# Optimization experiments

Hardware: AMD Instinct MI355X
Metric: run time of the kernel (lower is better)

Reference implementation:

```python
import jax, jax.numpy as jnp
import numpy as np

B, H, W, C = 2, 64, 64, 512
GROUPS = 32
EPS = 1e-5


def group_norm(x, gamma, beta):
    b, h, w, c = x.shape
    xg = x.reshape(b, h, w, GROUPS, c // GROUPS)
    mu = xg.mean(axis=(1, 2, 4), keepdims=True)
    var = xg.var(axis=(1, 2, 4), keepdims=True)
    xn = ((xg - mu) * jax.lax.rsqrt(var + EPS)).reshape(b, h, w, c)
    return xn * gamma + beta


def setup_inputs() -> dict:
    key = jax.random.key(0)
    ks = jax.random.split(key, 12)
    wscale = 0.02
    inputs = jax.random.normal(ks[0], (B, H, W, C), jnp.float32)
    gamma = jnp.ones((C,), jnp.float32)
    beta = jnp.zeros((C,), jnp.float32)
    Wq = jax.random.normal(ks[1], (C, C), jnp.float32) * wscale
    bq = jnp.zeros((C,), jnp.float32)
    Wk = jax.random.normal(ks[2], (C, C), jnp.float32) * wscale
    bk = jnp.zeros((C,), jnp.float32)
    Wv = jax.random.normal(ks[3], (C, C), jnp.float32) * wscale
    bv = jnp.zeros((C,), jnp.float32)
    Wp = jax.random.normal(ks[4], (C, C), jnp.float32) * wscale
    bp = jnp.zeros((C,), jnp.float32)
    return {"inputs": inputs, "gamma": gamma, "beta": beta,
            "Wq": Wq, "bq": bq, "Wk": Wk, "bk": bk,
            "Wv": Wv, "bv": bv, "Wp": Wp, "bp": bp}


def reference(inputs, gamma, beta, Wq, bq, Wk, bk, Wv, bv, Wp, bp):
    b, h, w, c = inputs.shape
    x = group_norm(inputs, gamma, beta)
    # QKV projections on [b, h, w, c], flatten spatial to sequence hw
    q = (x @ Wq + bq).reshape(b, h * w, c)
    k = (x @ Wk + bk).reshape(b, h * w, c)
    v = (x @ Wv + bv).reshape(b, h * w, c)
    scale = 1.0 / jnp.sqrt(jnp.asarray(c, q.dtype))
    # y[b,i,j] = <q_i, k_j> / sqrt(c); softmax over keys j (last axis, keras default)
    attn = jax.nn.softmax(jnp.einsum('bqc,bkc->bqk', q, k) * scale, axis=-1)
    # out_i = sum_j attn[i,j] * v_j  (matches v @ y^T in the original)
    o = jnp.einsum('bqk,bkc->bqc', attn, v).reshape(b, h, w, c)
    return (o @ Wp + bp) + inputs
```

## Files before the change

kernel.cpp:

```cpp
#include <hip/hip_runtime.h>
#include <hip/hip_bf16.h>
#include <cstddef>


typedef __bf16 bf16;
typedef __attribute__((ext_vector_type(8))) __bf16 bf16x8;
typedef __attribute__((ext_vector_type(4))) __bf16 bf16x4;
typedef __attribute__((ext_vector_type(4))) float f32x4;

#define SEQ   4096
#define CCH   512
#define NBAT  2

__global__ __launch_bounds__(256) void prep(
    const float* __restrict__ x,
    const float* __restrict__ Wq, const float* __restrict__ Wk,
    const float* __restrict__ Wv, const float* __restrict__ Wp,
    const float* __restrict__ bq, const float* __restrict__ bk,
    const float* __restrict__ bv,
    float* __restrict__ stats, bf16* __restrict__ WqkvT,
    bf16* __restrict__ WpT, float* __restrict__ biasQKV) {
    const int bid = blockIdx.x;
    if (bid < 512) {
        int bg = bid >> 3, c = bid & 7;
        int b = bg >> 5, g = bg & 31;
        const float* base = x + (size_t)b * SEQ * CCH + g * 16;
        float s = 0.f, ss = 0.f;
        for (int i = threadIdx.x; i < 2048; i += 256) {
            int sp = c * 512 + (i >> 2), q = i & 3;
            float4 v = *(const float4*)(base + (size_t)sp * CCH + q * 4);
            s  += v.x + v.y + v.z + v.w;
            ss += v.x * v.x + v.y * v.y + v.z * v.z + v.w * v.w;
        }
        #pragma unroll
        for (int o = 32; o > 0; o >>= 1) { s += __shfl_down(s, o); ss += __shfl_down(ss, o); }
        __shared__ float red[2][4];
        int wave = threadIdx.x >> 6, lane = threadIdx.x & 63;
        if (lane == 0) { red[0][wave] = s; red[1][wave] = ss; }
        __syncthreads();
        if (threadIdx.x == 0) {
            atomicAdd(&stats[bg * 2],     red[0][0] + red[0][1] + red[0][2] + red[0][3]);
            atomicAdd(&stats[bg * 2 + 1], red[1][0] + red[1][1] + red[1][2] + red[1][3]);
        }
    } else if (bid < 1536) {
        __shared__ float tile[32][33];
        int w = bid - 512;
        int z = w >> 8, rest = w & 255;
        int k0 = (rest >> 4) * 32, n0 = (rest & 15) * 32;
        const float* W = (z == 0) ? Wq : (z == 1) ? Wk : (z == 2) ? Wv : Wp;
        int tx = threadIdx.x & 31, ty = threadIdx.x >> 5;
        #pragma unroll
        for (int i = ty; i < 32; i += 8)
            tile[i][tx] = W[(size_t)(k0 + i) * CCH + n0 + tx];
        __syncthreads();
        bf16* dst = (z < 3) ? (WqkvT + (size_t)z * CCH * CCH) : WpT;
        #pragma unroll
        for (int i = ty; i < 32; i += 8)
            dst[(size_t)(n0 + i) * CCH + k0 + tx] = (bf16)tile[tx][i];
    } else {
        for (int i = threadIdx.x; i < 1536; i += 256) {
            float v = (i < 512) ? bq[i] : (i < 1024) ? bk[i - 512] : bv[i - 1024];
            biasQKV[i] = v;
        }
    }
}

__global__ __launch_bounds__(256) void gn_apply(const float* __restrict__ x,
                                                const float* __restrict__ stats,
                                                const float* __restrict__ gamma,
                                                const float* __restrict__ beta,
                                                bf16* __restrict__ xn) {
    size_t idx = (size_t)blockIdx.x * 256 + threadIdx.x;
    int c4 = (int)(idx & 127);
    size_t sb = idx >> 7;
    int b = (int)(sb >> 12);
    int g = c4 >> 2;
    int bg = b * 32 + g;
    float S = stats[bg * 2], SS = stats[bg * 2 + 1];
    float mu = S * (1.f / 65536.f);
    float rs = rsqrtf(SS * (1.f / 65536.f) - mu * mu + 1e-5f);
    float4 v  = ((const float4*)x)[idx];
    float4 gm = ((const float4*)gamma)[c4];
    float4 bt = ((const float4*)beta)[c4];
    bf16x4 o;
    o[0] = (bf16)((v.x - mu) * rs * gm.x + bt.x);
    o[1] = (bf16)((v.y - mu) * rs * gm.y + bt.y);
    o[2] = (bf16)((v.z - mu) * rs * gm.z + bt.z);
    o[3] = (bf16)((v.w - mu) * rs * gm.w + bt.w);
    ((bf16x4*)xn)[idx] = o;
}

template <int EPI, int BN>
__device__ __forceinline__ void gemm2_body(
    int bxi, int byi, int bzi,
    const bf16* __restrict__ A, long long aBatch, int lda,
    const bf16* __restrict__ Bt, long long bBatch, int ldb,
    void* __restrict__ Cout, long long cBatch, int ldc,
    int K, int bkmask, float scale,
    const float* __restrict__ bias, const float* __restrict__ resid,
    float* __restrict__ lsum, long long lsumBatch) {
    constexpr int JN = BN / 32;
    __shared__ __align__(16) bf16 As[128 * 64];
    __shared__ __align__(16) bf16 Bs[BN * 64];
    __shared__ float lscr[256];
    __shared__ float lrow[128];
    const int tid = threadIdx.x;
    const int lane = tid & 63;
    const int wave = tid >> 6;

    int zb = bzi, kc = 0;
    if constexpr (EPI == 2) { kc = zb & 1; zb >>= 1; }
    const long long m0 = (long long)bxi * 128;
    const long long n0 = (long long)byi * BN;
    const bf16* Ab = A + (long long)zb * aBatch + (EPI == 2 ? (long long)kc * 2048 : 0);
    const bf16* Bb = Bt + (long long)zb * bBatch + (EPI == 2 ? (long long)kc * 2048 : 0);

    if constexpr (EPI == 2) {
        const float* lsb = lsum + (long long)zb * lsumBatch + m0;
        const int row = tid & 127, h = tid >> 7;
        float s = 0.f;
        #pragma unroll
        for (int p = 0; p < 32; ++p)
            s += lsb[(long long)(h * 32 + p) * SEQ + row];
        lscr[tid] = s;
        __syncthreads();
        if (tid < 128) lrow[tid] = 1.f / (lscr[tid] + lscr[tid + 128]);
    }

    const int wm = (wave & 1) * 64;
    const int wn = (wave >> 1) * (BN / 2);
    const int fm = lane & 15;
    const int q4 = lane >> 4;

    f32x4 acc[4][JN];
    #pragma unroll
    for (int i = 0; i < 4; ++i)
        #pragma unroll
        for (int j = 0; j < JN; ++j)
            acc[i][j] = (f32x4){0.f, 0.f, 0.f, 0.f};

    const int srow = tid >> 3;
    const int schunk = (tid & 7) ^ (srow & 7);

    for (int k0 = 0; k0 < K; k0 += 64) {
        const int kA = k0 + schunk * 8;
        const int kB = (k0 & bkmask) + schunk * 8;
        #pragma unroll
        for (int cb = 0; cb < 4; ++cb) {
            const bf16* g = Ab + (m0 + cb * 32 + srow) * (long long)lda + kA;
            __builtin_amdgcn_global_load_lds((const __attribute__((address_space(1))) void*)g,
                                             (__attribute__((address_space(3))) void*)&As[cb * 2048 + tid * 8], 16, 0, 0);
        }
        #pragma unroll
        for (int cb = 0; cb < BN / 32; ++cb) {
            const bf16* g = Bb + (n0 + cb * 32 + srow) * (long long)ldb + kB;
            __builtin_amdgcn_global_load_lds((const __attribute__((address_space(1))) void*)g,
                                             (__attribute__((address_space(3))) void*)&Bs[cb * 2048 + tid * 8], 16, 0, 0);
        }
        __syncthreads();
        #pragma unroll
        for (int kcc = 0; kcc < 2; ++kcc) {
            bf16x8 fa[4], fb[JN];
            #pragma unroll
            for (int i = 0; i < 4; ++i) {
                const int row = wm + i * 16 + fm;
                const int sw = ((kcc * 4 + q4) ^ (fm & 7)) * 8;
                fa[i] = *(const bf16x8*)&As[row * 64 + sw];
            }
            #pragma unroll
            for (int j = 0; j < JN; ++j) {
                const int row = wn + j * 16 + fm;
                const int sw = ((kcc * 4 + q4) ^ (fm & 7)) * 8;
                fb[j] = *(const bf16x8*)&Bs[row * 64 + sw];
            }
            #pragma unroll
            for (int i = 0; i < 4; ++i)
                #pragma unroll
                for (int j = 0; j < JN; ++j)
                    acc[i][j] = __builtin_amdgcn_mfma_f32_16x16x32_bf16(fa[i], fb[j], acc[i][j], 0, 0, 0);
        }
        __syncthreads();
    }

    const int col = lane & 15;
    const int rowb = (lane >> 4) * 4;

    if constexpr (EPI == 1) {
        bf16* Pb = (bf16*)Cout + (long long)zb * cBatch;
        float* lsw = lsum + (long long)zb * lsumBatch
                   + ((long long)byi * 2 + (wave >> 1)) * SEQ;
        #pragma unroll
        for (int i = 0; i < 4; ++i) {
            float rs[4] = {0.f, 0.f, 0.f, 0.f};
            long long mg = m0 + wm + i * 16 + rowb;
            #pragma unroll
            for (int j = 0; j < JN; ++j) {
                long long ng = n0 + wn + j * 16 + col;
                #pragma unroll
                for (int r = 0; r < 4; ++r) {
                    float e = __expf(acc[i][j][r] * scale);
                    rs[r] += e;
                    Pb[(mg + r) * (long long)ldc + ng] = (bf16)e;
                }
            }
            #pragma unroll
            for (int r = 0; r < 4; ++r) {
                rs[r] += __shfl_xor(rs[r], 1);
                rs[r] += __shfl_xor(rs[r], 2);
                rs[r] += __shfl_xor(rs[r], 4);
                rs[r] += __shfl_xor(rs[r], 8);
            }
            if (col == 0) {
                #pragma unroll
                for (int r = 0; r < 4; ++r) lsw[mg + r] = rs[r];
            }
        }
    } else {
        #pragma unroll
        for (int i = 0; i < 4; ++i) {
            #pragma unroll
            for (int j = 0; j < JN; ++j) {
                long long mg = m0 + wm + i * 16 + rowb;
                long long ng = n0 + wn + j * 16 + col;
                #pragma unroll
                for (int r = 0; r < 4; ++r) {
                    float v = acc[i][j][r];
                    long long m = mg + r;
                    if constexpr (EPI == 0) {
                        ((bf16*)Cout)[m * (long long)ldc + ng] = (bf16)(v + bias[ng]);
                    } else if constexpr (EPI == 2) {
                        float inv = lrow[(int)(m - m0)];
                        ((bf16*)Cout)[(long long)zb * cBatch + m * (long long)ldc
                                      + kc * 512 + ng] = (bf16)(v * inv);
                    } else {
                        ((float*)Cout)[m * (long long)ldc + ng] =
                            v + bias[ng] + resid[m * CCH + ng];
                    }
                }
            }
        }
    }
}

template <int EPI, int BN>
__global__ __launch_bounds__(256, 2) void gemm2(
    const bf16* __restrict__ A, long long aBatch, int lda,
    const bf16* __restrict__ Bt, long long bBatch, int ldb,
    void* __restrict__ Cout, long long cBatch, int ldc,
    int K, int bkmask, float scale,
    const float* __restrict__ bias, const float* __restrict__ resid,
    float* __restrict__ lsum, long long lsumBatch) {
    gemm2_body<EPI, BN>(blockIdx.x, blockIdx.y, blockIdx.z,
                        A, aBatch, lda, Bt, bBatch, ldb, Cout, cBatch, ldc,
                        K, bkmask, scale, bias, resid, lsum, lsumBatch);
}

__device__ __forceinline__ void vtrans_body(const bf16* __restrict__ qkv,
                                            bf16* __restrict__ vT,
                                            int b, int s0, int c0) {
    __shared__ bf16 tile[64][65];
    const int tx = threadIdx.x & 63;
    const int w = threadIdx.x >> 6;
    #pragma unroll
    for (int i = 0; i < 16; ++i) {
        int row = w + i * 4;
        tile[row][tx] = qkv[((size_t)b * SEQ + s0 + row) * 1536 + 1024 + c0 + tx];
    }
    __syncthreads();
    #pragma unroll
    for (int i = 0; i < 16; ++i) {
        int row = w + i * 4;
        vT[((size_t)b * CCH + c0 + row) * SEQ + s0 + tx] = tile[tx][row];
    }
}

__global__ __launch_bounds__(256, 2) void qk_vtrans(
    const bf16* __restrict__ qkv, bf16* __restrict__ vT,
    bf16* __restrict__ P, float* __restrict__ lsum,
    float scale, int vtBlocks,
    long long qkBatch, long long pBatch, long long lsumBatch) {
    const int bid = blockIdx.x;
    if (bid < vtBlocks) {
        int b = bid >> 9;
        int r = bid & 511;
        vtrans_body(qkv, vT, b, (r >> 3) * 64, (r & 7) * 64);
    } else {
        int q = bid - vtBlocks;
        int bz = q >> 10;
        int r = q & 1023;
        gemm2_body<1, 128>(r >> 5, r & 31, bz,
                           qkv, qkBatch, 1536, qkv + 512, qkBatch, 1536,
                           P, pBatch, SEQ, CCH, 0x7FFFFFFF, scale,
                           nullptr, nullptr, lsum, lsumBatch);
    }
}

extern "C" void kernel_launch(void* const* d_in, const int* in_sizes, int n_in,
                              void* d_out, int out_size, void* d_ws, size_t ws_size,
                              hipStream_t stream) {
    const float* x     = (const float*)d_in[0];
    const float* gamma = (const float*)d_in[1];
    const float* beta  = (const float*)d_in[2];
    const float* Wq    = (const float*)d_in[3];
    const float* bq    = (const float*)d_in[4];
    const float* Wk    = (const float*)d_in[5];
    const float* bk    = (const float*)d_in[6];
    const float* Wv    = (const float*)d_in[7];
    const float* bv    = (const float*)d_in[8];
    const float* Wp    = (const float*)d_in[9];
    const float* bp    = (const float*)d_in[10];
    float* out = (float*)d_out;

    constexpr size_t OFF_STATS = 0;
    constexpr size_t OFF_BIAS  = 1024;
    constexpr size_t OFF_WQKVT = 8192;
    constexpr size_t OFF_WPT   = 1581056;
    constexpr size_t OFF_XN    = 2105344;
    constexpr size_t OFF_LSUM  = OFF_XN;
    constexpr size_t OFF_QKV   = 10493952;
    constexpr size_t OFF_O2    = OFF_QKV;
    constexpr size_t OFF_VT    = 35659776;
    constexpr size_t OFF_P     = 44048384;
    constexpr size_t NEED_FULL = OFF_P + (size_t)NBAT * SEQ * SEQ * 2;

    char* ws = (char*)d_ws;
    float* stats   = (float*)(ws + OFF_STATS);
    float* biasQKV = (float*)(ws + OFF_BIAS);
    bf16*  WqkvT   = (bf16*)(ws + OFF_WQKVT);
    bf16*  WpT     = (bf16*)(ws + OFF_WPT);
    bf16*  xn      = (bf16*)(ws + OFF_XN);
    float* lsum    = (float*)(ws + OFF_LSUM);
    bf16*  qkv     = (bf16*)(ws + OFF_QKV);
    bf16*  o2      = (bf16*)(ws + OFF_O2);
    bf16*  vT      = (bf16*)(ws + OFF_VT);
    bf16*  P       = (bf16*)(ws + OFF_P);

    const float scale = 0.044194173824159216f;
    const int NOMASK = 0x7FFFFFFF;

    hipMemsetAsync(ws + OFF_STATS, 0, 512, stream);
    prep<<<1537, 256, 0, stream>>>(x, Wq, Wk, Wv, Wp, bq, bk, bv,
                                   stats, WqkvT, WpT, biasQKV);
    gn_apply<<<4096, 256, 0, stream>>>(x, stats, gamma, beta, xn);
    gemm2<0, 128><<<dim3(64, 12, 1), 256, 0, stream>>>(
        xn, 0, CCH, WqkvT, 0, CCH, qkv, 0, 1536,
        CCH, NOMASK, 1.f, biasQKV, nullptr, nullptr, 0);

    if (ws_size >= NEED_FULL) {
        qk_vtrans<<<3072, 256, 0, stream>>>(
            qkv, vT, P, lsum, scale, 1024,
            (long long)SEQ * 1536, (long long)SEQ * SEQ, 64LL * SEQ);
        gemm2<2, 128><<<dim3(32, 4, NBAT * 2), 256, 0, stream>>>(
            P, (long long)SEQ * SEQ, SEQ, vT, (long long)CCH * SEQ, SEQ,
            o2, (long long)SEQ * 1024, 1024,
            2048, NOMASK, 1.f, nullptr, nullptr, lsum, 64LL * SEQ);
    } else {
        for (int b = 0; b < NBAT; ++b) {
            const bf16* qb = qkv + (long long)b * SEQ * 1536;
            qk_vtrans<<<1536, 256, 0, stream>>>(
                qb, vT + (long long)b * CCH * SEQ, P,
                lsum + (long long)b * 64 * SEQ, scale, 512, 0, 0, 0);
            gemm2<2, 128><<<dim3(32, 4, 2), 256, 0, stream>>>(
                P, 0, SEQ, vT + (long long)b * CCH * SEQ, 0, SEQ,
                o2 + (long long)b * SEQ * 1024, 0, 1024,
                2048, NOMASK, 1.f, nullptr, nullptr,
                lsum + (long long)b * 64 * SEQ, 0);
        }
    }

    gemm2<3, 64><<<dim3(64, 8, 1), 256, 0, stream>>>(
        o2, 0, 1024, WpT, 0, CCH, out, 0, CCH,
        1024, 511, 1.f, bp, x, nullptr, 0);
}
```

Baseline: 220.8 us.

## Fuse all stages into one persistent cooperative kernel with grid syncs

Replaces the sequence of separate kernel launches (memset, prep, group-norm apply, QKV GEMM, QK^T/V-transpose, PV GEMM, output projection) with a single cooperative kernel of 512 blocks that loops over work units per stage and uses grid-wide barriers between stages. The stats atomics and memset are replaced by per-chunk partial sums reduced once into a shared-memory mu/rstd table. Shared memory is unified into one buffer, and the PV epilogue's row-sum load now runs after the main loop. This targets launch gaps and the memset, at the cost of grid-sync overhead and persistent-loop scheduling with fixed occupancy.

```diff
diff --git a/kernel.cpp b/kernel.cpp
--- a/kernel.cpp
+++ b/kernel.cpp
@@ -1,6 +1,9 @@
 #include <hip/hip_runtime.h>
 #include <hip/hip_bf16.h>
+#include <hip/hip_cooperative_groups.h>
 #include <cstddef>
+
+namespace cg = cooperative_groups;
 
 
 typedef __bf16 bf16;
@@ -11,22 +14,25 @@
 #define SEQ   4096
 #define CCH   512
 #define NBAT  2
-
-__global__ __launch_bounds__(256) void prep(
-    const float* __restrict__ x,
+#define NOMASK 0x7FFFFFFF
+#define SMEM_BYTES 32768
+
+__device__ __forceinline__ void prep_unit(
+    char* smem, int bid, const float* __restrict__ x,
     const float* __restrict__ Wq, const float* __restrict__ Wk,
     const float* __restrict__ Wv, const float* __restrict__ Wp,
     const float* __restrict__ bq, const float* __restrict__ bk,
     const float* __restrict__ bv,
-    float* __restrict__ stats, bf16* __restrict__ WqkvT,
+    float* __restrict__ statsP, bf16* __restrict__ WqkvT,
     bf16* __restrict__ WpT, float* __restrict__ biasQKV) {
-    const int bid = blockIdx.x;
+    const int tid = threadIdx.x;
     if (bid < 512) {
+        float* red = (float*)smem;
         int bg = bid >> 3, c = bid & 7;
         int b = bg >> 5, g = bg & 31;
         const float* base = x + (size_t)b * SEQ * CCH + g * 16;
         float s = 0.f, ss = 0.f;
-        for (int i = threadIdx.x; i < 2048; i += 256) {
+        for (int i = tid; i < 2048; i += 256) {
             int sp = c * 512 + (i >> 2), q = i & 3;
             float4 v = *(const float4*)(base + (size_t)sp * CCH + q * 4);
             s  += v.x + v.y + v.z + v.w;
@@ -34,21 +40,21 @@
         }
         #pragma unroll
         for (int o = 32; o > 0; o >>= 1) { s += __shfl_down(s, o); ss += __shfl_down(ss, o); }
-        __shared__ float red[2][4];
-        int wave = threadIdx.x >> 6, lane = threadIdx.x & 63;
-        if (lane == 0) { red[0][wave] = s; red[1][wave] = ss; }
-        __syncthreads();
-        if (threadIdx.x == 0) {
-            atomicAdd(&stats[bg * 2],     red[0][0] + red[0][1] + red[0][2] + red[0][3]);
-            atomicAdd(&stats[bg * 2 + 1], red[1][0] + red[1][1] + red[1][2] + red[1][3]);
-        }
+        int wave = tid >> 6, lane = tid & 63;
+        if (lane == 0) { red[wave] = s; red[4 + wave] = ss; }
+        __syncthreads();
+        if (tid == 0) {
+            statsP[bg * 16 + c]     = red[0] + red[1] + red[2] + red[3];
+            statsP[bg * 16 + 8 + c] = red[4] + red[5] + red[6] + red[7];
+        }
+        __syncthreads();
     } else if (bid < 1536) {
-        __shared__ float tile[32][33];
+        float (*tile)[33] = (float(*)[33])smem;
         int w = bid - 512;
         int z = w >> 8, rest = w & 255;
         int k0 = (rest >> 4) * 32, n0 = (rest & 15) * 32;
         const float* W = (z == 0) ? Wq : (z == 1) ? Wk : (z == 2) ? Wv : Wp;
-        int tx = threadIdx.x & 31, ty = threadIdx.x >> 5;
+        int tx = tid & 31, ty = tid >> 5;
         #pragma unroll
         for (int i = ty; i < 32; i += 8)
             tile[i][tx] = W[(size_t)(k0 + i) * CCH + n0 + tx];
@@ -57,28 +63,39 @@
         #pragma unroll
         for (int i = ty; i < 32; i += 8)
             dst[(size_t)(n0 + i) * CCH + k0 + tx] = (bf16)tile[tx][i];
+        __syncthreads();
     } else {
-        for (int i = threadIdx.x; i < 1536; i += 256) {
+        for (int i = tid; i < 1536; i += 256) {
             float v = (i < 512) ? bq[i] : (i < 1024) ? bk[i - 512] : bv[i - 1024];
             biasQKV[i] = v;
         }
     }
 }
 
-__global__ __launch_bounds__(256) void gn_apply(const float* __restrict__ x,
-                                                const float* __restrict__ stats,
-                                                const float* __restrict__ gamma,
-                                                const float* __restrict__ beta,
-                                                bf16* __restrict__ xn) {
-    size_t idx = (size_t)blockIdx.x * 256 + threadIdx.x;
+__device__ __forceinline__ void gn_table(char* smem, const float* __restrict__ statsP) {
+    float* tbl = (float*)smem;
+    const int tid = threadIdx.x;
+    if (tid < 64) {
+        float S = 0.f, SS = 0.f;
+        #pragma unroll
+        for (int c = 0; c < 8; ++c) { S += statsP[tid * 16 + c]; SS += statsP[tid * 16 + 8 + c]; }
+        float mu = S * (1.f / 65536.f);
+        float rs = rsqrtf(SS * (1.f / 65536.f) - mu * mu + 1e-5f);
+        tbl[tid * 2] = mu; tbl[tid * 2 + 1] = rs;
+    }
+    __syncthreads();
+}
+
+__device__ __forceinline__ void gn_unit(
+    char* smem, int w, const float* __restrict__ x,
+    const float* __restrict__ gamma, const float* __restrict__ beta,
+    bf16* __restrict__ xn) {
+    const float* tbl = (const float*)smem;
+    size_t idx = (size_t)w * 256 + threadIdx.x;
     int c4 = (int)(idx & 127);
-    size_t sb = idx >> 7;
-    int b = (int)(sb >> 12);
-    int g = c4 >> 2;
-    int bg = b * 32 + g;
-    float S = stats[bg * 2], SS = stats[bg * 2 + 1];
-    float mu = S * (1.f / 65536.f);
-    float rs = rsqrtf(SS * (1.f / 65536.f) - mu * mu + 1e-5f);
+    int b = (int)(idx >> 19);
+    int bg = b * 32 + (c4 >> 2);
+    float mu = tbl[bg * 2], rs = tbl[bg * 2 + 1];
     float4 v  = ((const float4*)x)[idx];
     float4 gm = ((const float4*)gamma)[c4];
     float4 bt = ((const float4*)beta)[c4];
@@ -90,9 +107,30 @@
     ((bf16x4*)xn)[idx] = o;
 }
 
+__device__ __forceinline__ void vtrans_unit(char* smem,
+                                            const bf16* __restrict__ qkv,
+                                            bf16* __restrict__ vT,
+                                            int b, int s0, int c0) {
+    bf16 (*tile)[65] = (bf16(*)[65])smem;
+    const int tx = threadIdx.x & 63;
+    const int w = threadIdx.x >> 6;
+    #pragma unroll
+    for (int i = 0; i < 16; ++i) {
+        int row = w + i * 4;
+        tile[row][tx] = qkv[((size_t)b * SEQ + s0 + row) * 1536 + 1024 + c0 + tx];
+    }
+    __syncthreads();
+    #pragma unroll
+    for (int i = 0; i < 16; ++i) {
+        int row = w + i * 4;
+        vT[((size_t)b * CCH + c0 + row) * SEQ + s0 + tx] = tile[tx][row];
+    }
+    __syncthreads();
+}
+
 template <int EPI, int BN>
 __device__ __forceinline__ void gemm2_body(
-    int bxi, int byi, int bzi,
+    char* smem, int bxi, int byi, int bzi,
     const bf16* __restrict__ A, long long aBatch, int lda,
     const bf16* __restrict__ Bt, long long bBatch, int ldb,
     void* __restrict__ Cout, long long cBatch, int ldc,
@@ -100,10 +138,8 @@
     const float* __restrict__ bias, const float* __restrict__ resid,
     float* __restrict__ lsum, long long lsumBatch) {
     constexpr int JN = BN / 32;
-    __shared__ __align__(16) bf16 As[128 * 64];
-    __shared__ __align__(16) bf16 Bs[BN * 64];
-    __shared__ float lscr[256];
-    __shared__ float lrow[128];
+    bf16* As = (bf16*)smem;
+    bf16* Bs = (bf16*)(smem + 16384);
     const int tid = threadIdx.x;
     const int lane = tid & 63;
     const int wave = tid >> 6;
@@ -115,18 +151,6 @@
     const bf16* Ab = A + (long long)zb * aBatch + (EPI == 2 ? (long long)kc * 2048 : 0);
     const bf16* Bb = Bt + (long long)zb * bBatch + (EPI == 2 ? (long long)kc * 2048 : 0);
 
-    if constexpr (EPI == 2) {
-        const float* lsb = lsum + (long long)zb * lsumBatch + m0;
-        const int row = tid & 127, h = tid >> 7;
-        float s = 0.f;
-        #pragma unroll
-        for (int p = 0; p < 32; ++p)
-            s += lsb[(long long)(h * 32 + p) * SEQ + row];
-        lscr[tid] = s;
-        __syncthreads();
-        if (tid < 128) lrow[tid] = 1.f / (lscr[tid] + lscr[tid + 128]);
-    }
-
     const int wm = (wave & 1) * 64;
     const int wn = (wave >> 1) * (BN / 2);
     const int fm = lane & 15;
@@ -179,6 +203,21 @@
                 for (int j = 0; j < JN; ++j)
                     acc[i][j] = __builtin_amdgcn_mfma_f32_16x16x32_bf16(fa[i], fb[j], acc[i][j], 0, 0, 0);
         }
+        __syncthreads();
+    }
+
+    float* lrow = (float*)(smem + 1024);
+    if constexpr (EPI == 2) {
+        float* lscr = (float*)smem;
+        const float* lsb = lsum + (long long)zb * lsumBatch + m0;
+        const int row = tid & 127, h = tid >> 7;
+        float s = 0.f;
+        #pragma unroll
+        for (int p = 0; p < 32; ++p)
+            s += lsb[(long long)(h * 32 + p) * SEQ + row];
+        lscr[tid] = s;
+        __syncthreads();
+        if (tid < 128) lrow[tid] = 1.f / (lscr[tid] + lscr[tid + 128]);
         __syncthreads();
     }
 
@@ -242,55 +281,112 @@
     }
 }
 
+struct FusedArgs {
+    const float *x, *gamma, *beta, *Wq, *bq, *Wk, *bk, *Wv, *bv, *Wp, *bp;
+    float* out;
+    float* statsP; float* biasQKV; bf16* WqkvT; bf16* WpT; bf16* xn;
+    float* lsum; bf16* qkv; bf16* o2; bf16* vT; bf16* P;
+};
+
+__global__ __launch_bounds__(256, 2) void fused(FusedArgs a) {
+    cg::grid_group grid = cg::this_grid();
+    __shared__ __align__(16) char smem[SMEM_BYTES];
+    const int nb = gridDim.x;
+    const float scale = 0.044194173824159216f;
+
+    for (int w = blockIdx.x; w < 1537; w += nb)
+        prep_unit(smem, w, a.x, a.Wq, a.Wk, a.Wv, a.Wp, a.bq, a.bk, a.bv,
+                  a.statsP, a.WqkvT, a.WpT, a.biasQKV);
+    grid.sync();
+
+    gn_table(smem, a.statsP);
+    for (int w = blockIdx.x; w < 4096; w += nb)
+        gn_unit(smem, w, a.x, a.gamma, a.beta, a.xn);
+    grid.sync();
+
+    for (int w = blockIdx.x; w < 768; w += nb)
+        gemm2_body<0, 128>(smem, w & 63, w >> 6, 0,
+                           a.xn, 0, CCH, a.WqkvT, 0, CCH, a.qkv, 0, 1536,
+                           CCH, NOMASK, 1.f, a.biasQKV, nullptr, nullptr, 0);
+    grid.sync();
+
+    for (int w = blockIdx.x; w < 3072; w += nb) {
+        if (w < 1024) {
+            int b = w >> 9, r = w & 511;
+            vtrans_unit(smem, a.qkv, a.vT, b, (r >> 3) * 64, (r & 7) * 64);
+        } else {
+            int u = w - 1024;
+            int bz = u >> 10, r = u & 1023;
+            gemm2_body<1, 128>(smem, r >> 5, r & 31, bz,
+                               a.qkv, (long long)SEQ * 1536, 1536,
+                               a.qkv + 512, (long long)SEQ * 1536, 1536,
+                               a.P, (long long)SEQ * SEQ, SEQ,
+                               CCH, NOMASK, scale, nullptr, nullptr,
+                               a.lsum, 64LL * SEQ);
+        }
+    }
+    grid.sync();
+
+    for (int w = blockIdx.x; w < 512; w += nb)
+        gemm2_body<2, 128>(smem, w & 31, (w >> 5) & 3, w >> 7,
+                           a.P, (long long)SEQ * SEQ, SEQ,
+                           a.vT, (long long)CCH * SEQ, SEQ,
+                           a.o2, (long long)SEQ * 1024, 1024,
+                           2048, NOMASK, 1.f, nullptr, nullptr,
+                           a.lsum, 64LL * SEQ);
+    grid.sync();
+
+    for (int w = blockIdx.x; w < 512; w += nb)
+        gemm2_body<3, 64>(smem, w & 63, w >> 6, 0,
+                          a.o2, 0, 1024, a.WpT, 0, CCH, a.out, 0, CCH,
+                          1024, 511, 1.f, a.bp, a.x, nullptr, 0);
+}
+
+__global__ __launch_bounds__(256) void k_prep(
+    const float* x, const float* Wq, const float* Wk, const float* Wv,
+    const float* Wp, const float* bq, const float* bk, const float* bv,
+    float* statsP, bf16* WqkvT, bf16* WpT, float* biasQKV) {
+    __shared__ __align__(16) char smem[4352];
+    prep_unit(smem, blockIdx.x, x, Wq, Wk, Wv, Wp, bq, bk, bv,
+              statsP, WqkvT, WpT, biasQKV);
+}
+
+__global__ __launch_bounds__(256) void k_gn(
+    const float* x, const float* statsP, const float* gamma,
+    const float* beta, bf16* xn) {
+    __shared__ __align__(16) char smem[512];
+    gn_table(smem, statsP);
+    gn_unit(smem, blockIdx.x, x, gamma, beta, xn);
+}
+
 template <int EPI, int BN>
-__global__ __launch_bounds__(256, 2) void gemm2(
-    const bf16* __restrict__ A, long long aBatch, int lda,
-    const bf16* __restrict__ Bt, long long bBatch, int ldb,
-    void* __restrict__ Cout, long long cBatch, int ldc,
+__global__ __launch_bounds__(256, 2) void k_gemm2(
+    const bf16* A, long long aBatch, int lda,
+    const bf16* Bt, long long bBatch, int ldb,
+    void* Cout, long long cBatch, int ldc,
     int K, int bkmask, float scale,
-    const float* __restrict__ bias, const float* __restrict__ resid,
-    float* __restrict__ lsum, long long lsumBatch) {
-    gemm2_body<EPI, BN>(blockIdx.x, blockIdx.y, blockIdx.z,
+    const float* bias, const float* resid,
+    float* lsum, long long lsumBatch) {
+    __shared__ __align__(16) char smem[SMEM_BYTES];
+    gemm2_body<EPI, BN>(smem, blockIdx.x, blockIdx.y, blockIdx.z,
                         A, aBatch, lda, Bt, bBatch, ldb, Cout, cBatch, ldc,
                         K, bkmask, scale, bias, resid, lsum, lsumBatch);
 }
 
-__device__ __forceinline__ void vtrans_body(const bf16* __restrict__ qkv,
-                                            bf16* __restrict__ vT,
-                                            int b, int s0, int c0) {
-    __shared__ bf16 tile[64][65];
-    const int tx = threadIdx.x & 63;
-    const int w = threadIdx.x >> 6;
-    #pragma unroll
-    for (int i = 0; i < 16; ++i) {
-        int row = w + i * 4;
-        tile[row][tx] = qkv[((size_t)b * SEQ + s0 + row) * 1536 + 1024 + c0 + tx];
-    }
-    __syncthreads();
-    #pragma unroll
-    for (int i = 0; i < 16; ++i) {
-        int row = w + i * 4;
-        vT[((size_t)b * CCH + c0 + row) * SEQ + s0 + tx] = tile[tx][row];
-    }
-}
-
-__global__ __launch_bounds__(256, 2) void qk_vtrans(
-    const bf16* __restrict__ qkv, bf16* __restrict__ vT,
-    bf16* __restrict__ P, float* __restrict__ lsum,
-    float scale, int vtBlocks,
-    long long qkBatch, long long pBatch, long long lsumBatch) {
+__global__ __launch_bounds__(256, 2) void k_qk_vtrans(
+    const bf16* qkv, bf16* vT, bf16* P, float* lsum, float scale,
+    int vtBlocks, long long qkBatch, long long pBatch, long long lsumBatch) {
+    __shared__ __align__(16) char smem[SMEM_BYTES];
     const int bid = blockIdx.x;
     if (bid < vtBlocks) {
-        int b = bid >> 9;
-        int r = bid & 511;
-        vtrans_body(qkv, vT, b, (r >> 3) * 64, (r & 7) * 64);
+        int b = bid >> 9, r = bid & 511;
+        vtrans_unit(smem, qkv, vT, b, (r >> 3) * 64, (r & 7) * 64);
     } else {
         int q = bid - vtBlocks;
-        int bz = q >> 10;
-        int r = q & 1023;
-        gemm2_body<1, 128>(r >> 5, r & 31, bz,
+        int bz = q >> 10, r = q & 1023;
+        gemm2_body<1, 128>(smem, r >> 5, r & 31, bz,
                            qkv, qkBatch, 1536, qkv + 512, qkBatch, 1536,
-                           P, pBatch, SEQ, CCH, 0x7FFFFFFF, scale,
+                           P, pBatch, SEQ, CCH, NOMASK, scale,
                            nullptr, nullptr, lsum, lsumBatch);
     }
 }
@@ -312,19 +408,19 @@
     float* out = (float*)d_out;
 
     constexpr size_t OFF_STATS = 0;
-    constexpr size_t OFF_BIAS  = 1024;
-    constexpr size_t OFF_WQKVT = 8192;
-    constexpr size_t OFF_WPT   = 1581056;
-    constexpr size_t OFF_XN    = 2105344;
+    constexpr size_t OFF_BIAS  = 4096;
+    constexpr size_t OFF_WQKVT = 12288;
+    constexpr size_t OFF_WPT   = 1585152;
+    constexpr size_t OFF_XN    = 2109440;
     constexpr size_t OFF_LSUM  = OFF_XN;
-    constexpr size_t OFF_QKV   = 10493952;
+    constexpr size_t OFF_QKV   = 10498048;
     constexpr size_t OFF_O2    = OFF_QKV;
-    constexpr size_t OFF_VT    = 35659776;
-    constexpr size_t OFF_P     = 44048384;
+    constexpr size_t OFF_VT    = 35663872;
+    constexpr size_t OFF_P     = 44052480;
     constexpr size_t NEED_FULL = OFF_P + (size_t)NBAT * SEQ * SEQ * 2;
 
     char* ws = (char*)d_ws;
-    float* stats   = (float*)(ws + OFF_STATS);
+    float* statsP  = (float*)(ws + OFF_STATS);
     float* biasQKV = (float*)(ws + OFF_BIAS);
     bf16*  WqkvT   = (bf16*)(ws + OFF_WQKVT);
     bf16*  WpT     = (bf16*)(ws + OFF_WPT);
@@ -336,39 +432,56 @@
     bf16*  P       = (bf16*)(ws + OFF_P);
 
     const float scale = 0.044194173824159216f;
-    const int NOMASK = 0x7FFFFFFF;
-
-    hipMemsetAsync(ws + OFF_STATS, 0, 512, stream);
-    prep<<<1537, 256, 0, stream>>>(x, Wq, Wk, Wv, Wp, bq, bk, bv,
-                                   stats, WqkvT, WpT, biasQKV);
-    gn_apply<<<4096, 256, 0, stream>>>(x, stats, gamma, beta, xn);
-    gemm2<0, 128><<<dim3(64, 12, 1), 256, 0, stream>>>(
-        xn, 0, CCH, WqkvT, 0, CCH, qkv, 0, 1536,
-        CCH, NOMASK, 1.f, biasQKV, nullptr, nullptr, 0);
-
-    if (ws_size >= NEED_FULL) {
-        qk_vtrans<<<3072, 256, 0, stream>>>(
-            qkv, vT, P, lsum, scale, 1024,
-            (long long)SEQ * 1536, (long long)SEQ * SEQ, 64LL * SEQ);
-        gemm2<2, 128><<<dim3(32, 4, NBAT * 2), 256, 0, stream>>>(
-            P, (long long)SEQ * SEQ, SEQ, vT, (long long)CCH * SEQ, SEQ,
-            o2, (long long)SEQ * 1024, 1024,
-            2048, NOMASK, 1.f, nullptr, nullptr, lsum, 64LL * SEQ);
-    } else {
-        for (int b = 0; b < NBAT; ++b) {
-            const bf16* qb = qkv + (long long)b * SEQ * 1536;
-            qk_vtrans<<<1536, 256, 0, stream>>>(
-                qb, vT + (long long)b * CCH * SEQ, P,
-                lsum + (long long)b * 64 * SEQ, scale, 512, 0, 0, 0);
-            gemm2<2, 128><<<dim3(32, 4, 2), 256, 0, stream>>>(
-                P, 0, SEQ, vT + (long long)b * CCH * SEQ, 0, SEQ,
-                o2 + (long long)b * SEQ * 1024, 0, 1024,
-                2048, NOMASK, 1.f, nullptr, nullptr,
-                lsum + (long long)b * 64 * SEQ, 0);
-        }
-    }
-
-    gemm2<3, 64><<<dim3(64, 8, 1), 256, 0, stream>>>(
-        o2, 0, 1024, WpT, 0, CCH, out, 0, CCH,
-        1024, 511, 1.f, bp, x, nullptr, 0);
-}
+    const bool full = ws_size >= NEED_FULL;
+
+    bool coop = false;
+    if (full) {
+        int occ = 0;
+        hipError_t oe = hipOccupancyMaxActiveBlocksPerMultiprocessor(
+            &occ, (const void*)fused, 256, 0);
+        if (oe == hipSuccess && occ >= 2) {
+            FusedArgs a{x, gamma, beta, Wq, bq, Wk, bk, Wv, bv, Wp, bp, out,
+                        statsP, biasQKV, WqkvT, WpT, xn, lsum, qkv, o2, vT, P};
+            void* params[] = {&a};
+            hipError_t le = hipLaunchCooperativeKernel(
+                (const void*)fused, dim3(512), dim3(256), params, 0, stream);
+            if (le == hipSuccess) coop = true;
+            else (void)hipGetLastError();
+        } else {
+            (void)hipGetLastError();
+        }
+    }
+
+    if (!coop) {
+        k_prep<<<1537, 256, 0, stream>>>(x, Wq, Wk, Wv, Wp, bq, bk, bv,
+                                         statsP, WqkvT, WpT, biasQKV);
+        k_gn<<<4096, 256, 0, stream>>>(x, statsP, gamma, beta, xn);
+        k_gemm2<0, 128><<<dim3(64, 12, 1), 256, 0, stream>>>(
+            xn, 0, CCH, WqkvT, 0, CCH, qkv, 0, 1536,
+            CCH, NOMASK, 1.f, biasQKV, nullptr, nullptr, 0);
+        if (full) {
+            k_qk_vtrans<<<3072, 256, 0, stream>>>(
+                qkv, vT, P, lsum, scale, 1024,
+                (long long)SEQ * 1536, (long long)SEQ * SEQ, 64LL * SEQ);
+            k_gemm2<2, 128><<<dim3(32, 4, NBAT * 2), 256, 0, stream>>>(
+                P, (long long)SEQ * SEQ, SEQ, vT, (long long)CCH * SEQ, SEQ,
+                o2, (long long)SEQ * 1024, 1024,
+                2048, NOMASK, 1.f, nullptr, nullptr, lsum, 64LL * SEQ);
+        } else {
+            for (int b = 0; b < NBAT; ++b) {
+                const bf16* qb = qkv + (long long)b * SEQ * 1536;
+                k_qk_vtrans<<<1536, 256, 0, stream>>>(
+                    qb, vT + (long long)b * CCH * SEQ, P,
+                    lsum + (long long)b * 64 * SEQ, scale, 512, 0, 0, 0);
+                k_gemm2<2, 128><<<dim3(32, 4, 2), 256, 0, stream>>>(
+                    P, 0, SEQ, vT + (long long)b * CCH * SEQ, 0, SEQ,
+                    o2 + (long long)b * SEQ * 1024, 0, 1024,
+                    2048, NOMASK, 1.f, nullptr, nullptr,
+                    lsum + (long long)b * 64 * SEQ, 0);
+            }
+        }
+        k_gemm2<3, 64><<<dim3(64, 8, 1), 256, 0, stream>>>(
+            o2, 0, 1024, WpT, 0, CCH, out, 0, CCH,
+            1024, 511, 1.f, bp, x, nullptr, 0);
+    }
+}
```

After: 216.6 us. Within noise of the previous version (-1.9%).
